# Performance work log

Hardware: AMD Instinct MI355X
Metric: run time of the kernel (lower is better)

Reference implementation:

```python
import jax, jax.numpy as jnp
import numpy as np

B, S, D, H, F = 4, 2048, 512, 8, 2048
HD = D // H
EPS = 1e-5


def setup_inputs() -> dict:
    key = jax.random.key(0)
    ks = jax.random.split(key, 12)
    s = lambda fan_in: 1.0 / np.sqrt(fan_in)
    return {
        "x": jax.random.normal(ks[0], (B, S, D), dtype=jnp.float32),
        "Wqkv": jax.random.uniform(ks[1], (D, 3 * D), minval=-s(D), maxval=s(D)),
        "bqkv": jax.random.uniform(ks[2], (3 * D,), minval=-s(D), maxval=s(D)),
        "Wo": jax.random.uniform(ks[3], (D, D), minval=-s(D), maxval=s(D)),
        "bo": jax.random.uniform(ks[4], (D,), minval=-s(D), maxval=s(D)),
        "g1": jnp.ones((D,), jnp.float32),
        "beta1": jnp.zeros((D,), jnp.float32),
        "W1": jax.random.uniform(ks[5], (D, F), minval=-s(D), maxval=s(D)),
        "b1": jax.random.uniform(ks[6], (F,), minval=-s(D), maxval=s(D)),
        "W2": jax.random.uniform(ks[7], (F, D), minval=-s(F), maxval=s(F)),
        "b2": jax.random.uniform(ks[8], (D,), minval=-s(F), maxval=s(F)),
        "g2": jnp.ones((D,), jnp.float32),
        "beta2": jnp.zeros((D,), jnp.float32),
    }


def _layernorm(x, g, b):
    mu = jnp.mean(x, axis=-1, keepdims=True)
    var = jnp.mean(jnp.square(x - mu), axis=-1, keepdims=True)
    return (x - mu) * jax.lax.rsqrt(var + EPS) * g + b


def reference(x, Wqkv, bqkv, Wo, bo, g1, beta1, W1, b1, W2, b2, g2, beta2):
    b, s, d = x.shape
    # QKV projection -> [b, s, 3, H, HD] -> q,k,v each [b, H, s, HD]
    qkv = (x @ Wqkv + bqkv).reshape(b, s, 3, H, HD)
    q, k, v = jnp.moveaxis(qkv, 2, 0)            # [3, b, s, H, HD]
    q = q.transpose(0, 2, 1, 3)
    k = k.transpose(0, 2, 1, 3)
    v = v.transpose(0, 2, 1, 3)
    scores = jnp.einsum('bhqd,bhkd->bhqk', q, k) / np.sqrt(HD).astype(np.float32)
    attn = jax.nn.softmax(scores, axis=-1)
    ctx = jnp.einsum('bhqk,bhkd->bhqd', attn, v)
    ctx = ctx.transpose(0, 2, 1, 3).reshape(b, s, d)
    attn_out = ctx @ Wo + bo
    x = _layernorm(x + attn_out, g1, beta1)
    # FFN (dropout inactive in eval)
    ffn = jax.nn.relu(x @ W1 + b1) @ W2 + b2
    return _layernorm(x + ffn, g2, beta2)
```

## Files before the change

kernel.cpp:

```cpp
#include <hip/hip_runtime.h>
#include <hip/hip_bf16.h>

#define S_ 2048
#define M_ 8192

typedef __bf16 bf16x8 __attribute__((ext_vector_type(8)));
typedef float f32x4 __attribute__((ext_vector_type(4)));

__device__ __forceinline__ void gload16(const void* g, void* l) {
  __builtin_amdgcn_global_load_lds(
      (const __attribute__((address_space(1))) void*)g,
      (__attribute__((address_space(3))) void*)l, 16, 0, 0);
}

template<int CTRL>
__device__ __forceinline__ float dppf(float x) {
  return __int_as_float(__builtin_amdgcn_update_dpp(
      0, __float_as_int(x), CTRL, 0xF, 0xF, true));
}
__device__ __forceinline__ float red16_sum(float x) {
  x += dppf<0x121>(x);
  x += dppf<0x122>(x);
  x += dppf<0x124>(x);
  x += dppf<0x128>(x);
  return x;
}

__global__ __launch_bounds__(256)
void cvt_x_k(const float* __restrict__ x, __bf16* __restrict__ xb) {
  int i = blockIdx.x * 256 + threadIdx.x;
  float4 v = ((const float4*)x)[i];
  union { __bf16 hh[4]; uint2 u; } pk;
  pk.hh[0] = (__bf16)v.x; pk.hh[1] = (__bf16)v.y;
  pk.hh[2] = (__bf16)v.z; pk.hh[3] = (__bf16)v.w;
  ((uint2*)xb)[i] = pk.u;
}

__global__ __launch_bounds__(256)
void tcvt_k(const float* __restrict__ Wm, __bf16* __restrict__ Wt, int K, int N) {
  __shared__ float tile[64][65];
  int nbn = N >> 6;
  int tk = blockIdx.x / nbn, tn = blockIdx.x % nbn;
  int tc = threadIdx.x & 63, tr = threadIdx.x >> 6;
#pragma unroll
  for (int p = 0; p < 16; ++p) {
    int kl = p * 4 + tr;
    tile[kl][tc] = Wm[(size_t)(tk * 64 + kl) * N + tn * 64 + tc];
  }
  __syncthreads();
#pragma unroll
  for (int p = 0; p < 16; ++p) {
    int nl = p * 4 + tr;
    Wt[(size_t)(tn * 64 + nl) * K + tk * 64 + tc] = (__bf16)tile[tc][nl];
  }
}

template<int MODE, int N, int K, int BM>
__global__ __launch_bounds__(256, 2)
void gemm_k(const __bf16* __restrict__ A, const __bf16* __restrict__ Bt,
            const float* __restrict__ bias,
            float* __restrict__ outf, __bf16* __restrict__ outb,
            __bf16* __restrict__ outq, __bf16* __restrict__ outk,
            __bf16* __restrict__ outv) {
  constexpr int NB = N / 128;
  constexpr int BJ = (BM == 128) ? 4 : 2;
  __shared__ __bf16 As[BM * 64];
  __shared__ __bf16 Bs[128 * 64];

  int id = blockIdx.x;
  int cpx = gridDim.x >> 3;
  int sw = (id & 7) * cpx + (id >> 3);
  int mb = sw / NB, nb = sw % NB;

  int t = threadIdx.x;
  int lane = t & 63;
  int g = lane >> 4, c = lane & 15;
  int w = t >> 6;
  int wrow = (BM == 128) ? (w >> 1) * 64 : 0;
  int wcol = (BM == 128) ? (w & 1) * 64 : w * 32;

  const __bf16* Ab = A + (size_t)mb * BM * K;
  const __bf16* Bb = Bt + (size_t)nb * 128 * K;

  f32x4 acc[4][BJ] = {};

  for (int kt = 0; kt < K / 64; ++kt) {
#pragma unroll
    for (int it = 0; it < BM / 32; ++it) {
      int idx = it * 256 + t;
      int row = idx >> 3, ch = idx & 7;
      int sch = ch ^ (row & 7);
      gload16(Ab + (size_t)row * K + kt * 64 + sch * 8, (char*)As + idx * 16);
    }
#pragma unroll
    for (int it = 0; it < 4; ++it) {
      int idx = it * 256 + t;
      int row = idx >> 3, ch = idx & 7;
      int sch = ch ^ (row & 7);
      gload16(Bb + (size_t)row * K + kt * 64 + sch * 8, (char*)Bs + idx * 16);
    }
    __syncthreads();
#pragma unroll
    for (int kk = 0; kk < 2; ++kk) {
      bf16x8 af[4], bfv[BJ];
#pragma unroll
      for (int i = 0; i < 4; ++i) {
        int row = wrow + i * 16 + c;
        int ch = (kk * 4 + g) ^ (row & 7);
        af[i] = *(const bf16x8*)((const char*)As + row * 128 + ch * 16);
      }
#pragma unroll
      for (int j = 0; j < BJ; ++j) {
        int row = wcol + j * 16 + c;
        int ch = (kk * 4 + g) ^ (row & 7);
        bfv[j] = *(const bf16x8*)((const char*)Bs + row * 128 + ch * 16);
      }
      __builtin_amdgcn_s_setprio(1);
#pragma unroll
      for (int i = 0; i < 4; ++i)
#pragma unroll
        for (int j = 0; j < BJ; ++j)
          acc[i][j] = __builtin_amdgcn_mfma_f32_16x16x32_bf16(af[i], bfv[j],
                                                              acc[i][j], 0, 0, 0);
      __builtin_amdgcn_s_setprio(0);
    }
    __syncthreads();
  }

  int row0 = mb * BM + wrow;
  int col0 = nb * 128 + wcol;

  if (MODE == 1) {
#pragma unroll
    for (int j = 0; j < BJ; ++j) {
      int col = col0 + j * 16 + c;
      float bv = bias[col];
#pragma unroll
      for (int i = 0; i < 4; ++i)
#pragma unroll
        for (int r = 0; r < 4; ++r) {
          int rr = row0 + i * 16 + g * 4 + r;
          outf[(size_t)rr * N + col] = acc[i][j][r] + bv;
        }
    }
  } else if (MODE == 2 || MODE == 3) {
#pragma unroll
    for (int j = 0; j < BJ; ++j) {
      int col = col0 + j * 16 + c;
      float bv = bias[col];
#pragma unroll
      for (int i = 0; i < 4; ++i)
#pragma unroll
        for (int r = 0; r < 4; ++r) {
          int rr = row0 + i * 16 + g * 4 + r;
          float v = acc[i][j][r] + bv;
          if (MODE == 2) v = fmaxf(v, 0.f);
          outb[(size_t)rr * N + col] = (__bf16)v;
        }
    }
  } else {
    int tsel = nb >> 2;
    int h = ((nb & 3) << 1) | (w & 1);
#pragma unroll
    for (int j = 0; j < BJ; ++j) {
      int hd = j * 16 + c;
      float bv = bias[nb * 128 + wcol + j * 16 + c];
#pragma unroll
      for (int i = 0; i < 4; ++i) {
        int rr = row0 + i * 16 + g * 4;
        int b = rr >> 11, s = rr & 2047;
        int bh = b * 8 + h;
        if (tsel == 2) {
          union { __bf16 hh[4]; uint2 u; } pk;
#pragma unroll
          for (int r = 0; r < 4; ++r) pk.hh[r] = (__bf16)(acc[i][j][r] + bv);
          *(uint2*)(outv + ((size_t)bh * 64 + hd) * 2048 + s) = pk.u;
        } else {
          __bf16* dst = (tsel == 0 ? outq : outk);
#pragma unroll
          for (int r = 0; r < 4; ++r)
            dst[((size_t)bh * 2048 + s + r) * 64 + hd] = (__bf16)(acc[i][j][r] + bv);
        }
      }
    }
  }
}

__global__ __launch_bounds__(256, 4)
void attn_k(const __bf16* __restrict__ qb, const __bf16* __restrict__ kb,
            const __bf16* __restrict__ vt, __bf16* __restrict__ ctx) {
  __shared__ __bf16 Ks[2][64 * 64];
  __shared__ __bf16 Vs[2][64 * 64];
  __shared__ char P_lds[4][16 * 128];

  int id = blockIdx.x;
  int sw = (id & 7) * 128 + (id >> 3);
  int bh = sw >> 5, qblk = sw & 31;

  int t = threadIdx.x, lane = t & 63, w = t >> 6;
  int g = lane >> 4, c = lane & 15;

  const __bf16* Q  = qb + (size_t)bh * S_ * 64;
  const __bf16* Kp = kb + (size_t)bh * S_ * 64;
  const __bf16* Vp = vt + (size_t)bh * 64 * S_;

  int q0 = qblk * 64 + w * 16;

  bf16x8 qf[2];
#pragma unroll
  for (int kk = 0; kk < 2; ++kk) {
    bf16x8 v = *(const bf16x8*)(Q + (size_t)(q0 + c) * 64 + kk * 32 + g * 8);
#pragma unroll
    for (int e = 0; e < 8; ++e) v[e] = (__bf16)((float)v[e] * 0.18033688f);
    qf[kk] = v;
  }

  f32x4 o[4] = {};
  float srun[4] = {0.f, 0.f, 0.f, 0.f};

  char* Pw = P_lds[w];
  int kvoff[2];
#pragma unroll
  for (int kk = 0; kk < 2; ++kk)
    kvoff[kk] = c * 128 + ((kk * 4 + g) ^ (c & 7)) * 16;

  auto stage = [&](int kt, int buf) {
    int kbase = kt * 64;
#pragma unroll
    for (int it = 0; it < 2; ++it) {
      int idx = it * 256 + t;
      int row = idx >> 3, ch = idx & 7;
      int sch = ch ^ (row & 7);
      gload16(Kp + (size_t)(kbase + row) * 64 + sch * 8, (char*)Ks[buf] + idx * 16);
      gload16(Vp + (size_t)row * S_ + kbase + sch * 8,   (char*)Vs[buf] + idx * 16);
    }
  };

  stage(0, 0);

  auto step = [&](int kbi, int cur, bool last) {
    if (!last) stage(kbi + 1, cur ^ 1);
    if (last) asm volatile("s_waitcnt vmcnt(0)" ::: "memory");
    else      asm volatile("s_waitcnt vmcnt(4)" ::: "memory");
    __builtin_amdgcn_s_barrier();
    asm volatile("" ::: "memory");
    const char* Kb = (const char*)Ks[cur];
    const char* Vb = (const char*)Vs[cur];

    bf16x8 kf[4][2];
#pragma unroll
    for (int j = 0; j < 4; ++j)
#pragma unroll
      for (int kk = 0; kk < 2; ++kk)
        kf[j][kk] = *(const bf16x8*)(Kb + j * 2048 + kvoff[kk]);
    f32x4 sacc[4] = {};
    __builtin_amdgcn_s_setprio(1);
#pragma unroll
    for (int j = 0; j < 4; ++j) {
      sacc[j] = __builtin_amdgcn_mfma_f32_16x16x32_bf16(qf[0], kf[j][0], sacc[j], 0, 0, 0);
      sacc[j] = __builtin_amdgcn_mfma_f32_16x16x32_bf16(qf[1], kf[j][1], sacc[j], 0, 0, 0);
    }
    __builtin_amdgcn_s_setprio(0);

#pragma unroll
    for (int r = 0; r < 4; ++r) {
      float p0 = exp2f(sacc[0][r]);
      float p1 = exp2f(sacc[1][r]);
      float p2 = exp2f(sacc[2][r]);
      float p3 = exp2f(sacc[3][r]);
      srun[r] += (p0 + p1) + (p2 + p3);
      int prow = g * 4 + r;
      char* base = Pw + prow * 128;
      int sz = (prow & 7) << 4;
      *(__bf16*)(base + ((2 * c) ^ sz))      = (__bf16)p0;
      *(__bf16*)(base + ((32 + 2 * c) ^ sz)) = (__bf16)p1;
      *(__bf16*)(base + ((64 + 2 * c) ^ sz)) = (__bf16)p2;
      *(__bf16*)(base + ((96 + 2 * c) ^ sz)) = (__bf16)p3;
    }
#pragma unroll
    for (int kk = 0; kk < 2; ++kk) {
      int pch = (kk * 4 + g) ^ (c & 7);
      bf16x8 pf = *(const bf16x8*)(Pw + c * 128 + pch * 16);
      __builtin_amdgcn_s_setprio(1);
#pragma unroll
      for (int n = 0; n < 4; ++n) {
        bf16x8 vf = *(const bf16x8*)(Vb + n * 2048 + kvoff[kk]);
        o[n] = __builtin_amdgcn_mfma_f32_16x16x32_bf16(pf, vf, o[n], 0, 0, 0);
      }
      __builtin_amdgcn_s_setprio(0);
    }
    if (!last) {
      asm volatile("" ::: "memory");
      __builtin_amdgcn_s_barrier();
      asm volatile("" ::: "memory");
    }
  };

  for (int kbi = 0; kbi < 30; kbi += 2) {
    step(kbi, 0, false);
    step(kbi + 1, 1, false);
  }
  step(30, 0, false);
  step(31, 1, true);

  int b = bh >> 3, h = bh & 7;
  f32x4 inv;
#pragma unroll
  for (int r = 0; r < 4; ++r) inv[r] = 1.f / red16_sum(srun[r]);
#pragma unroll
  for (int n = 0; n < 4; ++n)
#pragma unroll
    for (int r = 0; r < 4; ++r) {
      int q = q0 + g * 4 + r;
      int d = n * 16 + c;
      ctx[((size_t)(b * 2048 + q)) * 512 + h * 64 + d] = (__bf16)(o[n][r] * inv[r]);
    }
}

template<bool IN1F32, bool WF>
__global__ __launch_bounds__(256)
void ln_k(const float* __restrict__ in1f, const __bf16* __restrict__ in1b,
          const __bf16* __restrict__ in2,
          const float* __restrict__ gam, const float* __restrict__ bet,
          float* __restrict__ outf, __bf16* __restrict__ outb) {
  int w = threadIdx.x >> 6, lane = threadIdx.x & 63;
  int row = blockIdx.x * 4 + w;
  size_t base = (size_t)row * 512 + lane * 8;
  float a[8];
  if (IN1F32) {
    float4 a0 = *(const float4*)(in1f + base);
    float4 a1 = *(const float4*)(in1f + base + 4);
    a[0] = a0.x; a[1] = a0.y; a[2] = a0.z; a[3] = a0.w;
    a[4] = a1.x; a[5] = a1.y; a[6] = a1.z; a[7] = a1.w;
  } else {
    bf16x8 av = *(const bf16x8*)(in1b + base);
#pragma unroll
    for (int k = 0; k < 8; ++k) a[k] = (float)av[k];
  }
  bf16x8 bv = *(const bf16x8*)(in2 + base);
  float x[8];
#pragma unroll
  for (int k = 0; k < 8; ++k) x[k] = a[k] + (float)bv[k];
  float s1 = 0.f, s2 = 0.f;
#pragma unroll
  for (int k = 0; k < 8; ++k) { s1 += x[k]; s2 += x[k] * x[k]; }
#pragma unroll
  for (int m = 1; m < 64; m <<= 1) { s1 += __shfl_xor(s1, m); s2 += __shfl_xor(s2, m); }
  float mu = s1 * (1.f / 512.f);
  float var = s2 * (1.f / 512.f) - mu * mu;
  float rs = rsqrtf(var + 1e-5f);
  float4 g0 = *(const float4*)(gam + lane * 8);
  float4 g1 = *(const float4*)(gam + lane * 8 + 4);
  float4 e0 = *(const float4*)(bet + lane * 8);
  float4 e1 = *(const float4*)(bet + lane * 8 + 4);
  float gg[8] = {g0.x, g0.y, g0.z, g0.w, g1.x, g1.y, g1.z, g1.w};
  float bb[8] = {e0.x, e0.y, e0.z, e0.w, e1.x, e1.y, e1.z, e1.w};
  float y[8];
#pragma unroll
  for (int k = 0; k < 8; ++k) y[k] = (x[k] - mu) * rs * gg[k] + bb[k];
  if (WF) {
    float4 o0 = {y[0], y[1], y[2], y[3]};
    float4 o1 = {y[4], y[5], y[6], y[7]};
    *(float4*)(outf + base) = o0;
    *(float4*)(outf + base + 4) = o1;
  } else {
    union { __bf16 hh[8]; uint4 u; } pk;
#pragma unroll
    for (int k = 0; k < 8; ++k) pk.hh[k] = (__bf16)y[k];
    *(uint4*)(outb + base) = pk.u;
  }
}

extern "C" void kernel_launch(void* const* d_in, const int* in_sizes, int n_in,
                              void* d_out, int out_size, void* d_ws, size_t ws_size,
                              hipStream_t stream) {
  (void)in_sizes; (void)n_in; (void)out_size;
  const float* x    = (const float*)d_in[0];
  const float* Wqkv = (const float*)d_in[1];
  const float* bqkv = (const float*)d_in[2];
  const float* Wo   = (const float*)d_in[3];
  const float* bo   = (const float*)d_in[4];
  const float* g1   = (const float*)d_in[5];
  const float* be1  = (const float*)d_in[6];
  const float* W1   = (const float*)d_in[7];
  const float* b1   = (const float*)d_in[8];
  const float* W2   = (const float*)d_in[9];
  const float* b2   = (const float*)d_in[10];
  const float* g2   = (const float*)d_in[11];
  const float* be2  = (const float*)d_in[12];
  float* out = (float*)d_out;

  char* ws = (char*)d_ws;
  size_t off = 0;
  auto alloc = [&](size_t bytes) {
    char* p = ws + off;
    off += (bytes + 255) & ~(size_t)255;
    return p;
  };
  __bf16* xb    = (__bf16*)alloc((size_t)M_ * 512 * 2);
  __bf16* wqkvt = (__bf16*)alloc((size_t)1536 * 512 * 2);
  __bf16* wot   = (__bf16*)alloc((size_t)512 * 512 * 2);
  __bf16* w1t   = (__bf16*)alloc((size_t)2048 * 512 * 2);
  __bf16* w2t   = (__bf16*)alloc((size_t)512 * 2048 * 2);
  __bf16* qbuf  = (__bf16*)alloc((size_t)32 * 2048 * 64 * 2);
  __bf16* kbuf  = (__bf16*)alloc((size_t)32 * 2048 * 64 * 2);
  __bf16* vtbuf = (__bf16*)alloc((size_t)32 * 64 * 2048 * 2);
  __bf16* ctxb  = (__bf16*)alloc((size_t)M_ * 512 * 2);
  __bf16* attnoutb = (__bf16*)alloc((size_t)M_ * 512 * 2);
  __bf16* y1b   = (__bf16*)alloc((size_t)M_ * 512 * 2);
  __bf16* h1    = (__bf16*)alloc((size_t)M_ * 2048 * 2);
  __bf16* f2b   = attnoutb;
  if (off > ws_size) return;

  cvt_x_k<<<4096, 256, 0, stream>>>(x, xb);
  tcvt_k<<<192, 256, 0, stream>>>(Wqkv, wqkvt, 512, 1536);
  tcvt_k<<<64, 256, 0, stream>>>(Wo, wot, 512, 512);
  tcvt_k<<<256, 256, 0, stream>>>(W1, w1t, 512, 2048);
  tcvt_k<<<256, 256, 0, stream>>>(W2, w2t, 2048, 512);

  gemm_k<0, 1536, 512, 128><<<768, 256, 0, stream>>>(xb, wqkvt, bqkv, nullptr, nullptr,
                                                     qbuf, kbuf, vtbuf);
  attn_k<<<1024, 256, 0, stream>>>(qbuf, kbuf, vtbuf, ctxb);
  gemm_k<3, 512, 512, 64><<<512, 256, 0, stream>>>(ctxb, wot, bo, nullptr, attnoutb,
                                                   nullptr, nullptr, nullptr);
  ln_k<true, false><<<2048, 256, 0, stream>>>(x, nullptr, attnoutb, g1, be1,
                                              nullptr, y1b);
  gemm_k<2, 2048, 512, 128><<<1024, 256, 0, stream>>>(y1b, w1t, b1, nullptr, h1,
                                                      nullptr, nullptr, nullptr);
  gemm_k<3, 512, 2048, 64><<<512, 256, 0, stream>>>(h1, w2t, b2, nullptr, f2b,
                                                    nullptr, nullptr, nullptr);
  ln_k<false, true><<<2048, 256, 0, stream>>>(nullptr, y1b, f2b, g2, be2,
                                              out, nullptr);
}
```

Before: 173.5 us.

## Split attention warps over query and key halves, keep P in registers

Each block's four waves now form a 2x2 grid: two query halves of 32 rows, each split across two key halves of 32 keys. S is computed transposed (K as the A operand) so the exp'd probabilities land directly in the register layout of the PV MFMA's A operand. This removes the LDS round-trip for P and its associated LDS traffic. The catch is that half of each PV MFMA's K dimension is zero-padded, and partial O and row sums must be reduced across waves through LDS at the end.

```diff
diff --git a/kernel.cpp b/kernel.cpp
--- a/kernel.cpp
+++ b/kernel.cpp
@@ -191,7 +191,7 @@
             const __bf16* __restrict__ vt, __bf16* __restrict__ ctx) {
   __shared__ __bf16 Ks[2][64 * 64];
   __shared__ __bf16 Vs[2][64 * 64];
-  __shared__ char P_lds[4][16 * 128];
+  __shared__ float srun_lds[2][2][16];
 
   int id = blockIdx.x;
   int sw = (id & 7) * 128 + (id >> 3);
@@ -199,30 +199,35 @@
 
   int t = threadIdx.x, lane = t & 63, w = t >> 6;
   int g = lane >> 4, c = lane & 15;
+  int wq = w >> 1, wk = w & 1;
 
   const __bf16* Q  = qb + (size_t)bh * S_ * 64;
   const __bf16* Kp = kb + (size_t)bh * S_ * 64;
   const __bf16* Vp = vt + (size_t)bh * 64 * S_;
 
-  int q0 = qblk * 64 + w * 16;
-
-  bf16x8 qf[2];
-#pragma unroll
-  for (int kk = 0; kk < 2; ++kk) {
-    bf16x8 v = *(const bf16x8*)(Q + (size_t)(q0 + c) * 64 + kk * 32 + g * 8);
-#pragma unroll
-    for (int e = 0; e < 8; ++e) v[e] = (__bf16)((float)v[e] * 0.18033688f);
-    qf[kk] = v;
-  }
-
-  f32x4 o[4] = {};
-  float srun[4] = {0.f, 0.f, 0.f, 0.f};
-
-  char* Pw = P_lds[w];
-  int kvoff[2];
-#pragma unroll
-  for (int kk = 0; kk < 2; ++kk)
-    kvoff[kk] = c * 128 + ((kk * 4 + g) ^ (c & 7)) * 16;
+  int q0 = qblk * 64;
+
+  bf16x8 qf[2][2];
+#pragma unroll
+  for (int i = 0; i < 2; ++i)
+#pragma unroll
+    for (int kk = 0; kk < 2; ++kk) {
+      bf16x8 v = *(const bf16x8*)(Q + (size_t)(q0 + wq * 32 + i * 16 + c) * 64 + kk * 32 + g * 8);
+#pragma unroll
+      for (int e = 0; e < 8; ++e) v[e] = (__bf16)((float)v[e] * 0.18033688f);
+      qf[i][kk] = v;
+    }
+
+  f32x4 o[2][4] = {};
+  float srun[2] = {0.f, 0.f};
+
+  int sz = c & 7;
+  int krow_base = (wk * 32 + c) * 128;
+  int kchunk[2] = { ((0 + g) ^ sz) * 16, ((4 + g) ^ sz) * 16 };
+  int vchunk[2];
+#pragma unroll
+  for (int j = 0; j < 2; ++j)
+    vchunk[j] = ((wk * 4 + j * 2 + (g >> 1)) ^ sz) * 16 + (g & 1) * 8;
 
   auto stage = [&](int kt, int buf) {
     int kbase = kt * 64;
@@ -237,6 +242,8 @@
   };
 
   stage(0, 0);
+
+  union PU { bf16x8 v; uint u[4]; };
 
   auto step = [&](int kbi, int cur, bool last) {
     if (!last) stage(kbi + 1, cur ^ 1);
@@ -247,48 +254,63 @@
     const char* Kb = (const char*)Ks[cur];
     const char* Vb = (const char*)Vs[cur];
 
-    bf16x8 kf[4][2];
-#pragma unroll
-    for (int j = 0; j < 4; ++j)
+    bf16x8 kf[2][2];
+#pragma unroll
+    for (int j = 0; j < 2; ++j)
 #pragma unroll
       for (int kk = 0; kk < 2; ++kk)
-        kf[j][kk] = *(const bf16x8*)(Kb + j * 2048 + kvoff[kk]);
-    f32x4 sacc[4] = {};
+        kf[j][kk] = *(const bf16x8*)(Kb + krow_base + j * 2048 + kchunk[kk]);
+
+    f32x4 sacc[2][2];
     __builtin_amdgcn_s_setprio(1);
 #pragma unroll
-    for (int j = 0; j < 4; ++j) {
-      sacc[j] = __builtin_amdgcn_mfma_f32_16x16x32_bf16(qf[0], kf[j][0], sacc[j], 0, 0, 0);
-      sacc[j] = __builtin_amdgcn_mfma_f32_16x16x32_bf16(qf[1], kf[j][1], sacc[j], 0, 0, 0);
-    }
+    for (int i = 0; i < 2; ++i)
+#pragma unroll
+      for (int j = 0; j < 2; ++j) {
+        f32x4 z = {};
+        z = __builtin_amdgcn_mfma_f32_16x16x32_bf16(kf[j][0], qf[i][0], z, 0, 0, 0);
+        sacc[i][j] = __builtin_amdgcn_mfma_f32_16x16x32_bf16(kf[j][1], qf[i][1], z, 0, 0, 0);
+      }
     __builtin_amdgcn_s_setprio(0);
 
-#pragma unroll
-    for (int r = 0; r < 4; ++r) {
-      float p0 = exp2f(sacc[0][r]);
-      float p1 = exp2f(sacc[1][r]);
-      float p2 = exp2f(sacc[2][r]);
-      float p3 = exp2f(sacc[3][r]);
-      srun[r] += (p0 + p1) + (p2 + p3);
-      int prow = g * 4 + r;
-      char* base = Pw + prow * 128;
-      int sz = (prow & 7) << 4;
-      *(__bf16*)(base + ((2 * c) ^ sz))      = (__bf16)p0;
-      *(__bf16*)(base + ((32 + 2 * c) ^ sz)) = (__bf16)p1;
-      *(__bf16*)(base + ((64 + 2 * c) ^ sz)) = (__bf16)p2;
-      *(__bf16*)(base + ((96 + 2 * c) ^ sz)) = (__bf16)p3;
-    }
-#pragma unroll
-    for (int kk = 0; kk < 2; ++kk) {
-      int pch = (kk * 4 + g) ^ (c & 7);
-      bf16x8 pf = *(const bf16x8*)(Pw + c * 128 + pch * 16);
-      __builtin_amdgcn_s_setprio(1);
-#pragma unroll
-      for (int n = 0; n < 4; ++n) {
-        bf16x8 vf = *(const bf16x8*)(Vb + n * 2048 + kvoff[kk]);
-        o[n] = __builtin_amdgcn_mfma_f32_16x16x32_bf16(pf, vf, o[n], 0, 0, 0);
-      }
-      __builtin_amdgcn_s_setprio(0);
-    }
+    PU vf[4][2];
+#pragma unroll
+    for (int n = 0; n < 4; ++n)
+#pragma unroll
+      for (int j = 0; j < 2; ++j) {
+        uint2 dv = *(const uint2*)(Vb + (n * 16 + c) * 128 + vchunk[j]);
+        vf[n][j].u[0] = dv.x; vf[n][j].u[1] = dv.y;
+        vf[n][j].u[2] = 0u;   vf[n][j].u[3] = 0u;
+      }
+
+    PU pf[2][2];
+#pragma unroll
+    for (int i = 0; i < 2; ++i)
+#pragma unroll
+      for (int j = 0; j < 2; ++j) {
+        float p0 = exp2f(sacc[i][j][0]);
+        float p1 = exp2f(sacc[i][j][1]);
+        float p2 = exp2f(sacc[i][j][2]);
+        float p3 = exp2f(sacc[i][j][3]);
+        srun[i] += (p0 + p1) + (p2 + p3);
+        union { __bf16 h[2]; uint u; } a, b;
+        a.h[0] = (__bf16)p0; a.h[1] = (__bf16)p1;
+        b.h[0] = (__bf16)p2; b.h[1] = (__bf16)p3;
+        pf[i][j].u[0] = a.u; pf[i][j].u[1] = b.u;
+        pf[i][j].u[2] = 0u;  pf[i][j].u[3] = 0u;
+      }
+
+    __builtin_amdgcn_s_setprio(1);
+#pragma unroll
+    for (int j = 0; j < 2; ++j)
+#pragma unroll
+      for (int n = 0; n < 4; ++n)
+#pragma unroll
+        for (int i = 0; i < 2; ++i)
+          o[i][n] = __builtin_amdgcn_mfma_f32_16x16x32_bf16(pf[i][j].v, vf[n][j].v,
+                                                            o[i][n], 0, 0, 0);
+    __builtin_amdgcn_s_setprio(0);
+
     if (!last) {
       asm volatile("" ::: "memory");
       __builtin_amdgcn_s_barrier();
@@ -303,18 +325,44 @@
   step(30, 0, false);
   step(31, 1, true);
 
-  int b = bh >> 3, h = bh & 7;
-  f32x4 inv;
-#pragma unroll
-  for (int r = 0; r < 4; ++r) inv[r] = 1.f / red16_sum(srun[r]);
-#pragma unroll
-  for (int n = 0; n < 4; ++n)
-#pragma unroll
-    for (int r = 0; r < 4; ++r) {
-      int q = q0 + g * 4 + r;
-      int d = n * 16 + c;
-      ctx[((size_t)(b * 2048 + q)) * 512 + h * 64 + d] = (__bf16)(o[n][r] * inv[r]);
-    }
+#pragma unroll
+  for (int i = 0; i < 2; ++i) {
+    srun[i] += __shfl_xor(srun[i], 16);
+    srun[i] += __shfl_xor(srun[i], 32);
+  }
+  __syncthreads();
+  float* olds = (float*)Ks;
+  if (wk == 1) {
+#pragma unroll
+    for (int i = 0; i < 2; ++i) {
+#pragma unroll
+      for (int n = 0; n < 4; ++n)
+#pragma unroll
+        for (int r = 0; r < 4; ++r)
+          olds[wq * 2048 + (i * 16 + g * 4 + r) * 64 + n * 16 + c] = o[i][n][r];
+      if (lane < 16) srun_lds[wq][i][c] = srun[i];
+    }
+  }
+  __syncthreads();
+  if (wk == 0) {
+    int b = bh >> 3, h = bh & 7;
+#pragma unroll
+    for (int i = 0; i < 2; ++i) {
+      float stot = srun[i] + srun_lds[wq][i][c];
+      float inv[4];
+#pragma unroll
+      for (int r = 0; r < 4; ++r)
+        inv[r] = 1.f / __shfl(stot, (lane & 48) | (g * 4 + r));
+#pragma unroll
+      for (int n = 0; n < 4; ++n)
+#pragma unroll
+        for (int r = 0; r < 4; ++r) {
+          float osum = o[i][n][r] + olds[wq * 2048 + (i * 16 + g * 4 + r) * 64 + n * 16 + c];
+          int q = q0 + wq * 32 + i * 16 + g * 4 + r;
+          ctx[((size_t)(b * 2048 + q)) * 512 + h * 64 + n * 16 + c] = (__bf16)(osum * inv[r]);
+        }
+    }
+  }
 }
 
 template<bool IN1F32, bool WF>
```

Result: slower. 268.4 us (+54.7%).

## Double-buffer GEMM LDS tiles to overlap global loads with MFMA

Applied to the files above, without the earlier changes.

The GEMM kernel now keeps two LDS buffers for the A and B tiles and issues the next k-tile's global-to-LDS loads before computing on the current one. Partial vmcnt waits replace the full __syncthreads, so only the current tile's loads must land before the barrier. This hides global load latency behind MFMA work. In exchange LDS use doubles, and the launch bound for BM=64 is raised to 3 blocks per CU, which limits registers per thread and may cause spills.

```diff
diff --git a/kernel.cpp b/kernel.cpp
--- a/kernel.cpp
+++ b/kernel.cpp
@@ -56,7 +56,7 @@
 }
 
 template<int MODE, int N, int K, int BM>
-__global__ __launch_bounds__(256, 2)
+__global__ __launch_bounds__(256, (BM == 128) ? 2 : 3)
 void gemm_k(const __bf16* __restrict__ A, const __bf16* __restrict__ Bt,
             const float* __restrict__ bias,
             float* __restrict__ outf, __bf16* __restrict__ outb,
@@ -64,8 +64,10 @@
             __bf16* __restrict__ outv) {
   constexpr int NB = N / 128;
   constexpr int BJ = (BM == 128) ? 4 : 2;
-  __shared__ __bf16 As[BM * 64];
-  __shared__ __bf16 Bs[128 * 64];
+  constexpr int KT = K / 64;
+  constexpr int NLD = BM / 32 + 4;
+  __shared__ __bf16 As[2][BM * 64];
+  __shared__ __bf16 Bs[2][128 * 64];
 
   int id = blockIdx.x;
   int cpx = gridDim.x >> 3;
@@ -84,22 +86,36 @@
 
   f32x4 acc[4][BJ] = {};
 
-  for (int kt = 0; kt < K / 64; ++kt) {
+  auto stage = [&](int kt, int buf) {
 #pragma unroll
     for (int it = 0; it < BM / 32; ++it) {
       int idx = it * 256 + t;
       int row = idx >> 3, ch = idx & 7;
       int sch = ch ^ (row & 7);
-      gload16(Ab + (size_t)row * K + kt * 64 + sch * 8, (char*)As + idx * 16);
+      gload16(Ab + (size_t)row * K + kt * 64 + sch * 8, (char*)As[buf] + idx * 16);
     }
 #pragma unroll
     for (int it = 0; it < 4; ++it) {
       int idx = it * 256 + t;
       int row = idx >> 3, ch = idx & 7;
       int sch = ch ^ (row & 7);
-      gload16(Bb + (size_t)row * K + kt * 64 + sch * 8, (char*)Bs + idx * 16);
-    }
-    __syncthreads();
+      gload16(Bb + (size_t)row * K + kt * 64 + sch * 8, (char*)Bs[buf] + idx * 16);
+    }
+  };
+
+  stage(0, 0);
+
+  for (int kt = 0; kt < KT; ++kt) {
+    int cur = kt & 1;
+    bool last = (kt == KT - 1);
+    if (!last) stage(kt + 1, cur ^ 1);
+    if (last)          asm volatile("s_waitcnt vmcnt(0)" ::: "memory");
+    else if (NLD == 8) asm volatile("s_waitcnt vmcnt(8)" ::: "memory");
+    else               asm volatile("s_waitcnt vmcnt(6)" ::: "memory");
+    __builtin_amdgcn_s_barrier();
+    asm volatile("" ::: "memory");
+    const char* Al = (const char*)As[cur];
+    const char* Bl = (const char*)Bs[cur];
 #pragma unroll
     for (int kk = 0; kk < 2; ++kk) {
       bf16x8 af[4], bfv[BJ];
@@ -107,13 +123,13 @@
       for (int i = 0; i < 4; ++i) {
         int row = wrow + i * 16 + c;
         int ch = (kk * 4 + g) ^ (row & 7);
-        af[i] = *(const bf16x8*)((const char*)As + row * 128 + ch * 16);
+        af[i] = *(const bf16x8*)(Al + row * 128 + ch * 16);
       }
 #pragma unroll
       for (int j = 0; j < BJ; ++j) {
         int row = wcol + j * 16 + c;
         int ch = (kk * 4 + g) ^ (row & 7);
-        bfv[j] = *(const bf16x8*)((const char*)Bs + row * 128 + ch * 16);
+        bfv[j] = *(const bf16x8*)(Bl + row * 128 + ch * 16);
       }
       __builtin_amdgcn_s_setprio(1);
 #pragma unroll
@@ -124,7 +140,11 @@
                                                               acc[i][j], 0, 0, 0);
       __builtin_amdgcn_s_setprio(0);
     }
-    __syncthreads();
+    if (!last) {
+      asm volatile("" ::: "memory");
+      __builtin_amdgcn_s_barrier();
+      asm volatile("" ::: "memory");
+    }
   }
 
   int row0 = mb * BM + wrow;
```

Result: slower. 179.4 us (+3.4%).

## Split-K the N=512 output GEMMs and sum partials in layernorm

Applied to the files above, without the earlier changes.

Adds a split-K template parameter to the GEMM so the Wo and W2 projections each launch twice as many blocks, with each half of K writing a bf16 partial to its own buffer (bias only on the first). The layernorm kernels read the extra partial and add it before normalizing, so no separate reduction pass is needed. The aim is better occupancy on the 512-wide GEMMs, which previously launched only 512 blocks. In exchange it writes and reads one extra M×512 bf16 buffer per GEMM and rounds partial sums to bf16 before adding them.

```diff
diff --git a/kernel.cpp b/kernel.cpp
--- a/kernel.cpp
+++ b/kernel.cpp
@@ -55,7 +55,7 @@
   }
 }
 
-template<int MODE, int N, int K, int BM>
+template<int MODE, int N, int K, int BM, int KS = 1>
 __global__ __launch_bounds__(256, 2)
 void gemm_k(const __bf16* __restrict__ A, const __bf16* __restrict__ Bt,
             const float* __restrict__ bias,
@@ -64,12 +64,15 @@
             __bf16* __restrict__ outv) {
   constexpr int NB = N / 128;
   constexpr int BJ = (BM == 128) ? 4 : 2;
+  constexpr int KT = K / KS / 64;
   __shared__ __bf16 As[BM * 64];
   __shared__ __bf16 Bs[128 * 64];
 
   int id = blockIdx.x;
   int cpx = gridDim.x >> 3;
   int sw = (id & 7) * cpx + (id >> 3);
+  int ks = 0;
+  if (KS == 2) { ks = sw & 1; sw >>= 1; }
   int mb = sw / NB, nb = sw % NB;
 
   int t = threadIdx.x;
@@ -79,12 +82,12 @@
   int wrow = (BM == 128) ? (w >> 1) * 64 : 0;
   int wcol = (BM == 128) ? (w & 1) * 64 : w * 32;
 
-  const __bf16* Ab = A + (size_t)mb * BM * K;
-  const __bf16* Bb = Bt + (size_t)nb * 128 * K;
+  const __bf16* Ab = A + (size_t)mb * BM * K + (size_t)ks * (K / KS);
+  const __bf16* Bb = Bt + (size_t)nb * 128 * K + (size_t)ks * (K / KS);
 
   f32x4 acc[4][BJ] = {};
 
-  for (int kt = 0; kt < K / 64; ++kt) {
+  for (int kt = 0; kt < KT; ++kt) {
 #pragma unroll
     for (int it = 0; it < BM / 32; ++it) {
       int idx = it * 256 + t;
@@ -144,10 +147,11 @@
         }
     }
   } else if (MODE == 2 || MODE == 3) {
+    __bf16* dst = (KS == 2 && ks == 1) ? outq : outb;
 #pragma unroll
     for (int j = 0; j < BJ; ++j) {
       int col = col0 + j * 16 + c;
-      float bv = bias[col];
+      float bv = (KS == 2 && ks == 1) ? 0.f : bias[col];
 #pragma unroll
       for (int i = 0; i < 4; ++i)
 #pragma unroll
@@ -155,7 +159,7 @@
           int rr = row0 + i * 16 + g * 4 + r;
           float v = acc[i][j][r] + bv;
           if (MODE == 2) v = fmaxf(v, 0.f);
-          outb[(size_t)rr * N + col] = (__bf16)v;
+          dst[(size_t)rr * N + col] = (__bf16)v;
         }
     }
   } else {
@@ -317,10 +321,10 @@
     }
 }
 
-template<bool IN1F32, bool WF>
+template<bool IN1F32, bool WF, bool IN3>
 __global__ __launch_bounds__(256)
 void ln_k(const float* __restrict__ in1f, const __bf16* __restrict__ in1b,
-          const __bf16* __restrict__ in2,
+          const __bf16* __restrict__ in2, const __bf16* __restrict__ in3,
           const float* __restrict__ gam, const float* __restrict__ bet,
           float* __restrict__ outf, __bf16* __restrict__ outb) {
   int w = threadIdx.x >> 6, lane = threadIdx.x & 63;
@@ -341,6 +345,11 @@
   float x[8];
 #pragma unroll
   for (int k = 0; k < 8; ++k) x[k] = a[k] + (float)bv[k];
+  if (IN3) {
+    bf16x8 cv = *(const bf16x8*)(in3 + base);
+#pragma unroll
+    for (int k = 0; k < 8; ++k) x[k] += (float)cv[k];
+  }
   float s1 = 0.f, s2 = 0.f;
 #pragma unroll
   for (int k = 0; k < 8; ++k) { s1 += x[k]; s2 += x[k] * x[k]; }
@@ -406,10 +415,10 @@
   __bf16* kbuf  = (__bf16*)alloc((size_t)32 * 2048 * 64 * 2);
   __bf16* vtbuf = (__bf16*)alloc((size_t)32 * 64 * 2048 * 2);
   __bf16* ctxb  = (__bf16*)alloc((size_t)M_ * 512 * 2);
-  __bf16* attnoutb = (__bf16*)alloc((size_t)M_ * 512 * 2);
+  __bf16* part0 = (__bf16*)alloc((size_t)M_ * 512 * 2);
+  __bf16* part1 = (__bf16*)alloc((size_t)M_ * 512 * 2);
   __bf16* y1b   = (__bf16*)alloc((size_t)M_ * 512 * 2);
   __bf16* h1    = (__bf16*)alloc((size_t)M_ * 2048 * 2);
-  __bf16* f2b   = attnoutb;
   if (off > ws_size) return;
 
   cvt_x_k<<<4096, 256, 0, stream>>>(x, xb);
@@ -421,14 +430,14 @@
   gemm_k<0, 1536, 512, 128><<<768, 256, 0, stream>>>(xb, wqkvt, bqkv, nullptr, nullptr,
                                                      qbuf, kbuf, vtbuf);
   attn_k<<<1024, 256, 0, stream>>>(qbuf, kbuf, vtbuf, ctxb);
-  gemm_k<3, 512, 512, 64><<<512, 256, 0, stream>>>(ctxb, wot, bo, nullptr, attnoutb,
-                                                   nullptr, nullptr, nullptr);
-  ln_k<true, false><<<2048, 256, 0, stream>>>(x, nullptr, attnoutb, g1, be1,
-                                              nullptr, y1b);
+  gemm_k<3, 512, 512, 64, 2><<<1024, 256, 0, stream>>>(ctxb, wot, bo, nullptr, part0,
+                                                       part1, nullptr, nullptr);
+  ln_k<true, false, true><<<2048, 256, 0, stream>>>(x, nullptr, part0, part1, g1, be1,
+                                                    nullptr, y1b);
   gemm_k<2, 2048, 512, 128><<<1024, 256, 0, stream>>>(y1b, w1t, b1, nullptr, h1,
                                                       nullptr, nullptr, nullptr);
-  gemm_k<3, 512, 2048, 64><<<512, 256, 0, stream>>>(h1, w2t, b2, nullptr, f2b,
-                                                    nullptr, nullptr, nullptr);
-  ln_k<false, true><<<2048, 256, 0, stream>>>(nullptr, y1b, f2b, g2, be2,
-                                              out, nullptr);
-}
+  gemm_k<3, 512, 2048, 64, 2><<<1024, 256, 0, stream>>>(h1, w2t, b2, nullptr, part0,
+                                                        part1, nullptr, nullptr);
+  ln_k<false, true, true><<<2048, 256, 0, stream>>>(nullptr, y1b, part0, part1, g2, be2,
+                                                    out, nullptr);
+}
```

After: 168.6 us. -2.8%, faster.
